# Kernel optimization log

Hardware: AMD Instinct MI355X
Metric: run time of the kernel (lower is better)

Reference implementation:

```python
import jax, jax.numpy as jnp
import numpy as np

B, D = 65536, 365

def _linp(k, fan_in, fan_out):
    # torch nn.Linear default init: U(-1/sqrt(fan_in), 1/sqrt(fan_in))
    kw, kb = jax.random.split(k)
    bound = 1.0 / np.sqrt(fan_in)
    W = jax.random.uniform(kw, (fan_in, fan_out), jnp.float32, -bound, bound)
    b = jax.random.uniform(kb, (fan_out,), jnp.float32, -bound, bound)
    return W, b

def setup_inputs() -> dict:
    key = jax.random.key(0)
    ks = jax.random.split(key, 9)
    x = jax.random.normal(ks[0], (B, D), jnp.float32)
    W1, b1 = _linp(ks[1], D, 512)
    W2, b2 = _linp(ks[2], 512, 256)
    W3, b3 = _linp(ks[3], 256, 128)
    Ws, bs = _linp(ks[4], 6, 32)
    Wc1, bc1 = _linp(ks[5], 128 + 32, 64)
    Wc2, bc2 = _linp(ks[6], 64, 32)
    Wc3, bc3 = _linp(ks[7], 32, 1)
    return dict(x=x, W1=W1, b1=b1, W2=W2, b2=b2, W3=W3, b3=b3,
                Ws=Ws, bs=bs, Wc1=Wc1, bc1=bc1, Wc2=Wc2, bc2=bc2,
                Wc3=Wc3, bc3=bc3)

def _row_stats(x):
    # fused row-wise moments: mean, std (ddof=1), min, max, skew, kurtosis
    mu = jnp.mean(x, axis=1, keepdims=True)          # [B,1]
    c = x - mu                                        # [B,D]
    var1 = jnp.sum(c * c, axis=1) / (x.shape[1] - 1)  # unbiased, matches torch.std()
    sigma = jnp.sqrt(var1)
    m3 = jnp.mean(c ** 3, axis=1)
    m4 = jnp.mean(c ** 4, axis=1)
    skew = m3 / (sigma ** 3 + 1e-8)
    kurt = m4 / (sigma ** 4 + 1e-8)
    return jnp.stack([mu[:, 0], sigma, jnp.min(x, axis=1), jnp.max(x, axis=1), skew, kurt], axis=1)

def reference(x, W1, b1, W2, b2, W3, b3, Ws, bs, Wc1, bc1, Wc2, bc2, Wc3, bc3):
    h = jax.nn.relu(x @ W1 + b1)
    h = jax.nn.relu(h @ W2 + b2)
    seq = jax.nn.relu(h @ W3 + b3)            # [B,128]
    stat = _row_stats(x) @ Ws + bs            # [B,32]
    comb = jnp.concatenate([seq, stat], axis=1)
    c = jax.nn.relu(comb @ Wc1 + bc1)
    c = jax.nn.relu(c @ Wc2 + bc2)
    out = jax.nn.sigmoid(c @ Wc3 + bc3)       # [B,1]
    return out[:, 0]
```

## Files before the change

### kernel.cpp

```cpp
#include <hip/hip_runtime.h>
#include <math.h>

typedef __attribute__((ext_vector_type(8)))  short short8;
typedef __attribute__((ext_vector_type(16))) float float16;

#define DEVI __device__ __forceinline__

DEVI short f2bf(float f) {
    unsigned u = __float_as_uint(f);
    u = (u + 0x7fffu + ((u >> 16) & 1u)) >> 16;
    return (short)u;
}
DEVI unsigned pk2(float a, float b) {
    return (unsigned)(unsigned short)f2bf(a) | ((unsigned)(unsigned short)f2bf(b) << 16);
}
DEVI float16 mfma16(short8 a, short8 b, float16 c) {
    return __builtin_amdgcn_mfma_f32_32x32x16_bf16(a, b, c, 0, 0, 0);
}
DEVI int rowof(int r, int h) { return (r & 3) + 8 * (r >> 2) + 4 * h; }
DEVI short8 lds8(const short* p) { return *(const short8*)p; }
DEVI short8 gld8(const short* p) { return *(const short8*)p; }

#define W1T_OFF  0
#define W2T_OFF  188416
#define W3T_OFF  319488
#define WC1T_OFF 352256
#define WC2T_OFF 362496

__global__ void prep_v2(const float* __restrict__ W1, const float* __restrict__ W2,
                        const float* __restrict__ W3, const float* __restrict__ Wc1,
                        const float* __restrict__ Wc2, short* __restrict__ ws) {
    __shared__ short T[16 * 72];
    int b = blockIdx.x, t = threadIdx.x;
    const float* src; int K, N; size_t base; int kc, nb;
    if (b < 184)        {            src = W1;  K = 365; N = 512; base = W1T_OFF;  kc = b >> 3;  nb = b & 7; }
    else if (b < 312)   { int l = b - 184; src = W2;  K = 512; N = 256; base = W2T_OFF;  kc = l >> 2;  nb = l & 3; }
    else if (b < 344)   { int l = b - 312; src = W3;  K = 256; N = 128; base = W3T_OFF;  kc = l >> 1;  nb = l & 1; }
    else if (b < 354)   {            src = Wc1; K = 160; N = 64;  base = WC1T_OFF; kc = b - 344; nb = 0; }
    else                {            src = Wc2; K = 64;  N = 32;  base = WC2T_OFF; kc = b - 354; nb = 0; }
    int n = nb * 64 + (t & 63);
    int kr = t >> 6;
    #pragma unroll
    for (int i = 0; i < 4; ++i) {
        int krow = kr + 4 * i;
        int k = kc * 16 + krow;
        float v = (k < K && n < N) ? src[(size_t)k * N + n] : 0.f;
        T[krow * 72 + (t & 63)] = f2bf(v);
    }
    __syncthreads();
    int n2 = t >> 2, ksq = (t & 3) * 4;
    int ng = nb * 64 + n2;
    if (ng < N) {
        unsigned lo = (unsigned)(unsigned short)T[ksq * 72 + n2]
                    | ((unsigned)(unsigned short)T[(ksq + 1) * 72 + n2] << 16);
        unsigned hi = (unsigned)(unsigned short)T[(ksq + 2) * 72 + n2]
                    | ((unsigned)(unsigned short)T[(ksq + 3) * 72 + n2] << 16);
        uint2 d; d.x = lo; d.y = hi;
        *(uint2*)(ws + base + ((size_t)kc * N + ng) * 16 + ksq) = d;
    }
}

__global__ __launch_bounds__(256, 2)
void fused_v5(const float* __restrict__ x,
              const float* __restrict__ b1f, const float* __restrict__ b2f,
              const float* __restrict__ b3f, const float* __restrict__ Wsf,
              const float* __restrict__ bsf, const float* __restrict__ bc1f,
              const float* __restrict__ bc2f, const float* __restrict__ Wc3f,
              const float* __restrict__ bc3f,
              const short* __restrict__ wsw, float* __restrict__ out)
{
    __shared__ __align__(16) char smem[53248];
    short* XT    = (short*)smem;
    short* SB0   = (short*)smem;
    short* SB1   = (short*)(smem + 17408);
    float* C2f   = (float*)(smem + 36864);
    short* FEATL = (short*)(smem + 48128);

    const short* W1t  = wsw + W1T_OFF;
    const short* W2t  = wsw + W2T_OFF;
    const short* W3t  = wsw + W3T_OFF;
    const short* Wc1t = wsw + WC1T_OFF;
    const short* Wc2t = wsw + WC2T_OFF;

    const int tid  = (int)threadIdx.x;
    const int lane = tid & 63;
    const int wv   = tid >> 6;
    const int m    = lane & 31;
    const int h    = lane >> 5;
    const int rowBase = (int)blockIdx.x * 64;

    float bb1[2][2], bb2[2];
    #pragma unroll
    for (int p = 0; p < 2; ++p)
    #pragma unroll
    for (int ct = 0; ct < 2; ++ct) bb1[p][ct] = b1f[256 * p + 64 * wv + 32 * ct + m];
    bb2[0] = b2f[64 * wv + m]; bb2[1] = b2f[64 * wv + 32 + m];
    float bb3  = b3f[32 * wv + m];
    float bbc1 = bc1f[32 * (wv & 1) + m];
    float bbc2 = bc2f[m];

    const int r0 = tid >> 2, q = tid & 2 ? (tid & 3) : (tid & 3);
    const int qq = tid & 3;
    const float* xrow = x + (size_t)(rowBase + r0) * 365;
    float s1 = 0.f, s2 = 0.f, s3 = 0.f, s4 = 0.f, mn = 1e30f, mx = -1e30f;
    #pragma unroll
    for (int i = 0; i < 12; ++i) {
        int o = qq + 4 * i;
        if (o <= 45) {
            float xf[8];
            #pragma unroll
            for (int jj = 0; jj < 8; ++jj) {
                int col = o * 8 + jj;
                xf[jj] = (col < 365) ? xrow[col] : 0.f;
            }
            #pragma unroll
            for (int jj = 0; jj < 8; ++jj) {
                int col = o * 8 + jj;
                if (col < 365) {
                    float v = xf[jj], v2 = v * v;
                    s1 += v; s2 += v2; s3 += v2 * v; s4 += v2 * v2;
                    mn = fminf(mn, v); mx = fmaxf(mx, v);
                }
            }
            int4 w4;
            w4.x = (int)pk2(xf[0], xf[1]); w4.y = (int)pk2(xf[2], xf[3]);
            w4.z = (int)pk2(xf[4], xf[5]); w4.w = (int)pk2(xf[6], xf[7]);
            *(int4*)(XT + r0 * 376 + o * 8) = w4;
        }
    }
    #pragma unroll
    for (int off = 1; off <= 2; off <<= 1) {
        s1 += __shfl_xor(s1, off); s2 += __shfl_xor(s2, off);
        s3 += __shfl_xor(s3, off); s4 += __shfl_xor(s4, off);
        mn = fminf(mn, __shfl_xor(mn, off)); mx = fmaxf(mx, __shfl_xor(mx, off));
    }
    {
        float mean  = s1 * (1.0f / 365.0f);
        float var1  = (s2 - 365.0f * mean * mean) * (1.0f / 364.0f);
        float sigma = sqrtf(var1);
        float m3 = (s3 - 3.0f * mean * s2) * (1.0f / 365.0f) + 2.0f * mean * mean * mean;
        float mm = mean * mean;
        float m4 = (s4 - 4.0f * mean * s3 + 6.0f * mm * s2) * (1.0f / 365.0f) - 3.0f * mm * mm;
        float sg2 = sigma * sigma;
        float skew = m3 / (sigma * sg2 + 1e-8f);
        float kurt = m4 / (sg2 * sg2 + 1e-8f);
        float st[6] = { mean, sigma, mn, mx, skew, kurt };
        float f[8];
        #pragma unroll
        for (int c0 = 0; c0 < 8; ++c0) {
            int c = 8 * qq + c0;
            float acc = bsf[c];
            #pragma unroll
            for (int jj = 0; jj < 6; ++jj) acc += st[jj] * Wsf[jj * 32 + c];
            f[c0] = acc;
        }
        int4 w4;
        w4.x = (int)pk2(f[0], f[1]); w4.y = (int)pk2(f[2], f[3]);
        w4.z = (int)pk2(f[4], f[5]); w4.w = (int)pk2(f[6], f[7]);
        *(int4*)(FEATL + r0 * 40 + 8 * qq) = w4;
    }
    __syncthreads();

    const short* Ap0 = XT + m * 376 + h * 8;
    const short* Ap1 = Ap0 + 32 * 376;
    unsigned park[2][2][2][8];
    #pragma unroll
    for (int p = 0; p < 2; ++p) {
        float16 c00, c01, c10, c11;
        #pragma unroll
        for (int i = 0; i < 16; ++i) { c00[i] = 0.f; c01[i] = 0.f; c10[i] = 0.f; c11[i] = 0.f; }
        const short* B1 = W1t + (256 * p + 64 * wv + m) * 16 + h * 8;
        #pragma unroll
        for (int kc = 0; kc < 23; ++kc) {
            short8 b0 = gld8(B1 + kc * 8192);
            short8 b1 = gld8(B1 + 512 + kc * 8192);
            short8 a0 = lds8(Ap0 + kc * 16);
            short8 a1 = lds8(Ap1 + kc * 16);
            c00 = mfma16(a0, b0, c00);
            c01 = mfma16(a1, b0, c01);
            c10 = mfma16(a0, b1, c10);
            c11 = mfma16(a1, b1, c11);
        }
        #pragma unroll
        for (int rr = 0; rr < 8; ++rr) {
            park[p][0][0][rr] = pk2(fmaxf(c00[2*rr] + bb1[p][0], 0.f), fmaxf(c00[2*rr+1] + bb1[p][0], 0.f));
            park[p][0][1][rr] = pk2(fmaxf(c01[2*rr] + bb1[p][0], 0.f), fmaxf(c01[2*rr+1] + bb1[p][0], 0.f));
            park[p][1][0][rr] = pk2(fmaxf(c10[2*rr] + bb1[p][1], 0.f), fmaxf(c10[2*rr+1] + bb1[p][1], 0.f));
            park[p][1][1][rr] = pk2(fmaxf(c11[2*rr] + bb1[p][1], 0.f), fmaxf(c11[2*rr+1] + bb1[p][1], 0.f));
        }
    }
    __syncthreads();

    float16 H00, H01, H10, H11;
    #pragma unroll
    for (int i = 0; i < 16; ++i) { H00[i] = 0.f; H01[i] = 0.f; H10[i] = 0.f; H11[i] = 0.f; }
    const short* A2r0 = SB0 + m * 136 + h * 8;
    #pragma unroll
    for (int s = 0; s < 4; ++s) {
        short* SBs = (s & 1) ? SB1 : SB0;
        if ((wv >> 1) == (s & 1)) {
            int p = s >> 1;
            int cb = 64 * (wv & 1) + m;
            #pragma unroll
            for (int ct = 0; ct < 2; ++ct)
            #pragma unroll
            for (int rt = 0; rt < 2; ++rt)
            #pragma unroll
            for (int rr = 0; rr < 8; ++rr) {
                unsigned pv = park[p][ct][rt][rr];
                int row = rt * 32 + rowof(2 * rr, h);
                SBs[row * 136 + cb + 32 * ct]       = (short)(pv & 0xffffu);
                SBs[(row + 1) * 136 + cb + 32 * ct] = (short)(pv >> 16);
            }
        }
        __syncthreads();
        const short* A0p = SBs + m * 136 + h * 8;
        const short* A1p = A0p + 32 * 136;
        const short* B2 = W2t + (64 * wv + m) * 16 + h * 8 + s * 32768;
        #pragma unroll
        for (int i = 0; i < 8; ++i) {
            short8 b0 = gld8(B2 + i * 4096);
            short8 b1 = gld8(B2 + 512 + i * 4096);
            short8 a0 = lds8(A0p + i * 16);
            short8 a1 = lds8(A1p + i * 16);
            H00 = mfma16(a0, b0, H00);
            H01 = mfma16(a1, b0, H01);
            H10 = mfma16(a0, b1, H10);
            H11 = mfma16(a1, b1, H11);
        }
    }
    (void)A2r0;

    float16 S0, S1;
    #pragma unroll
    for (int i = 0; i < 16; ++i) { S0[i] = 0.f; S1[i] = 0.f; }
    #pragma unroll
    for (int t = 0; t < 2; ++t) {
        short* SBs = t ? SB1 : SB0;
        if ((wv >> 1) == t) {
            int cb = 64 * (wv & 1) + m;
            #pragma unroll
            for (int rr = 0; rr < 8; ++rr) {
                int rw0 = rowof(2 * rr, h);
                SBs[rw0 * 136 + cb]              = f2bf(fmaxf(H00[2*rr]   + bb2[0], 0.f));
                SBs[(rw0 + 1) * 136 + cb]        = f2bf(fmaxf(H00[2*rr+1] + bb2[0], 0.f));
                SBs[(32 + rw0) * 136 + cb]       = f2bf(fmaxf(H01[2*rr]   + bb2[0], 0.f));
                SBs[(33 + rw0) * 136 + cb]       = f2bf(fmaxf(H01[2*rr+1] + bb2[0], 0.f));
                SBs[rw0 * 136 + cb + 32]         = f2bf(fmaxf(H10[2*rr]   + bb2[1], 0.f));
                SBs[(rw0 + 1) * 136 + cb + 32]   = f2bf(fmaxf(H10[2*rr+1] + bb2[1], 0.f));
                SBs[(32 + rw0) * 136 + cb + 32]  = f2bf(fmaxf(H11[2*rr]   + bb2[1], 0.f));
                SBs[(33 + rw0) * 136 + cb + 32]  = f2bf(fmaxf(H11[2*rr+1] + bb2[1], 0.f));
            }
        }
        __syncthreads();
        const short* A0p = SBs + m * 136 + h * 8;
        const short* A1p = A0p + 32 * 136;
        const short* B3 = W3t + (32 * wv + m) * 16 + h * 8 + t * 16384;
        #pragma unroll
        for (int i = 0; i < 8; ++i) {
            short8 b  = gld8(B3 + i * 2048);
            short8 a0 = lds8(A0p + i * 16);
            short8 a1 = lds8(A1p + i * 16);
            S0 = mfma16(a0, b, S0);
            S1 = mfma16(a1, b, S1);
        }
    }

    {
        int cb = 32 * wv + m;
        #pragma unroll
        for (int rr = 0; rr < 8; ++rr) {
            int rw0 = rowof(2 * rr, h);
            SB0[rw0 * 136 + cb]        = f2bf(fmaxf(S0[2*rr]   + bb3, 0.f));
            SB0[(rw0 + 1) * 136 + cb]  = f2bf(fmaxf(S0[2*rr+1] + bb3, 0.f));
            SB0[(32 + rw0) * 136 + cb] = f2bf(fmaxf(S1[2*rr]   + bb3, 0.f));
            SB0[(33 + rw0) * 136 + cb] = f2bf(fmaxf(S1[2*rr+1] + bb3, 0.f));
        }
    }
    __syncthreads();

    {
        int rt4 = wv >> 1, c4 = wv & 1;
        float16 g4;
        #pragma unroll
        for (int i = 0; i < 16; ++i) g4[i] = 0.f;
        const short* A4 = SB0 + (rt4 * 32 + m) * 136 + h * 8;
        const short* B4 = Wc1t + (32 * c4 + m) * 16 + h * 8;
        #pragma unroll
        for (int i = 0; i < 8; ++i)
            g4 = mfma16(lds8(A4 + i * 16), gld8(B4 + i * 1024), g4);
        const short* AF = FEATL + (rt4 * 32 + m) * 40 + h * 8;
        #pragma unroll
        for (int i = 0; i < 2; ++i)
            g4 = mfma16(lds8(AF + i * 16), gld8(B4 + (8 + i) * 1024), g4);
        short* C1 = SB1;
        #pragma unroll
        for (int r = 0; r < 16; ++r)
            C1[(rt4 * 32 + rowof(r, h)) * 72 + 32 * c4 + m] = f2bf(fmaxf(g4[r] + bbc1, 0.f));
    }
    __syncthreads();

    if (wv < 2) {
        const short* A5 = SB1 + (32 * wv + m) * 72 + h * 8;
        const short* B5 = Wc2t + m * 16 + h * 8;
        float16 g5;
        #pragma unroll
        for (int i = 0; i < 16; ++i) g5[i] = 0.f;
        #pragma unroll
        for (int i = 0; i < 4; ++i)
            g5 = mfma16(lds8(A5 + i * 16), gld8(B5 + i * 512), g5);
        #pragma unroll
        for (int r = 0; r < 16; ++r)
            C2f[(32 * wv + rowof(r, h)) * 33 + m] = fmaxf(g5[r] + bbc2, 0.f);
    }
    __syncthreads();

    if (tid < 64) {
        float z = bc3f[0];
        #pragma unroll
        for (int i = 0; i < 32; ++i) z += C2f[tid * 33 + i] * Wc3f[i];
        out[rowBase + tid] = 1.0f / (1.0f + expf(-z));
    }
}

extern "C" void kernel_launch(void* const* d_in, const int* in_sizes, int n_in,
                              void* d_out, int out_size, void* d_ws, size_t ws_size,
                              hipStream_t stream)
{
    (void)in_sizes; (void)n_in; (void)out_size; (void)ws_size;
    const float* x   = (const float*)d_in[0];
    const float* W1  = (const float*)d_in[1];
    const float* b1  = (const float*)d_in[2];
    const float* W2  = (const float*)d_in[3];
    const float* b2  = (const float*)d_in[4];
    const float* W3  = (const float*)d_in[5];
    const float* b3  = (const float*)d_in[6];
    const float* Ws  = (const float*)d_in[7];
    const float* bs  = (const float*)d_in[8];
    const float* Wc1 = (const float*)d_in[9];
    const float* bc1 = (const float*)d_in[10];
    const float* Wc2 = (const float*)d_in[11];
    const float* bc2 = (const float*)d_in[12];
    const float* Wc3 = (const float*)d_in[13];
    const float* bc3 = (const float*)d_in[14];
    short* ws = (short*)d_ws;

    prep_v2<<<358, 256, 0, stream>>>(W1, W2, W3, Wc1, Wc2, ws);
    fused_v5<<<1024, 256, 0, stream>>>(x, b1, b2, b3, Ws, bs, bc1, bc2, Wc3, bc3,
                                       ws, (float*)d_out);
}
```

Baseline: 245.5 us.

## Coalesce x row loads per wave and raise occupancy bound to three blocks

Replaces the per-thread strided load of x (four threads per row, each reading eight scalar columns) with a per-wave scheme in which each wave handles 16 rows and lanes read consecutive columns. Loads are therefore coalesced, and row moments are reduced with a full 64-lane shuffle tree. The bf16 packing now uses a neighbour shuffle, and the stat projection computes one output column per lane. The launch bound also rises from 2 to 3 blocks per SM, which gives more latency hiding but may force register spills given the large park/accumulator arrays.

```diff
diff --git a/kernel.cpp b/kernel.cpp
--- a/kernel.cpp
+++ b/kernel.cpp
@@ -60,8 +60,8 @@
     }
 }
 
-__global__ __launch_bounds__(256, 2)
-void fused_v5(const float* __restrict__ x,
+__global__ __launch_bounds__(256, 3)
+void fused_v6(const float* __restrict__ x,
               const float* __restrict__ b1f, const float* __restrict__ b2f,
               const float* __restrict__ b3f, const float* __restrict__ Wsf,
               const float* __restrict__ bsf, const float* __restrict__ bc1f,
@@ -98,43 +98,50 @@
     float bb3  = b3f[32 * wv + m];
     float bbc1 = bc1f[32 * (wv & 1) + m];
     float bbc2 = bc2f[m];
-
-    const int r0 = tid >> 2, q = tid & 2 ? (tid & 3) : (tid & 3);
-    const int qq = tid & 3;
-    const float* xrow = x + (size_t)(rowBase + r0) * 365;
-    float s1 = 0.f, s2 = 0.f, s3 = 0.f, s4 = 0.f, mn = 1e30f, mx = -1e30f;
-    #pragma unroll
-    for (int i = 0; i < 12; ++i) {
-        int o = qq + 4 * i;
-        if (o <= 45) {
-            float xf[8];
-            #pragma unroll
-            for (int jj = 0; jj < 8; ++jj) {
-                int col = o * 8 + jj;
-                xf[jj] = (col < 365) ? xrow[col] : 0.f;
-            }
-            #pragma unroll
-            for (int jj = 0; jj < 8; ++jj) {
-                int col = o * 8 + jj;
-                if (col < 365) {
-                    float v = xf[jj], v2 = v * v;
-                    s1 += v; s2 += v2; s3 += v2 * v; s4 += v2 * v2;
-                    mn = fminf(mn, v); mx = fmaxf(mx, v);
-                }
-            }
-            int4 w4;
-            w4.x = (int)pk2(xf[0], xf[1]); w4.y = (int)pk2(xf[2], xf[3]);
-            w4.z = (int)pk2(xf[4], xf[5]); w4.w = (int)pk2(xf[6], xf[7]);
-            *(int4*)(XT + r0 * 376 + o * 8) = w4;
-        }
-    }
-    #pragma unroll
-    for (int off = 1; off <= 2; off <<= 1) {
-        s1 += __shfl_xor(s1, off); s2 += __shfl_xor(s2, off);
-        s3 += __shfl_xor(s3, off); s4 += __shfl_xor(s4, off);
-        mn = fminf(mn, __shfl_xor(mn, off)); mx = fmaxf(mx, __shfl_xor(mx, off));
-    }
-    {
+    float wsf[6], bsl = bsf[m];
+    #pragma unroll
+    for (int j = 0; j < 6; ++j) wsf[j] = Wsf[j * 32 + m];
+
+    #pragma unroll
+    for (int i = 0; i < 16; ++i) {
+        int r = wv * 16 + i;
+        const float* xr = x + (size_t)(rowBase + r) * 365;
+        float v[6];
+        #pragma unroll
+        for (int t = 0; t < 5; ++t) v[t] = xr[64 * t + lane];
+        v[5] = (lane < 45) ? xr[320 + lane] : 0.f;
+
+        float s1 = 0.f, s2 = 0.f, s3 = 0.f, s4 = 0.f, mnr = 1e30f, mxr = -1e30f;
+        #pragma unroll
+        for (int t = 0; t < 5; ++t) {
+            float vv = v[t], v2 = vv * vv;
+            s1 += vv; s2 += v2; s3 += v2 * vv; s4 += v2 * v2;
+            mnr = fminf(mnr, vv); mxr = fmaxf(mxr, vv);
+        }
+        {
+            float vv = v[5], v2 = vv * vv;
+            s1 += vv; s2 += v2; s3 += v2 * vv; s4 += v2 * v2;
+            if (lane < 45) { mnr = fminf(mnr, vv); mxr = fmaxf(mxr, vv); }
+        }
+        unsigned pv[6];
+        #pragma unroll
+        for (int t = 0; t < 6; ++t) {
+            float vh = __shfl_xor(v[t], 1);
+            pv[t] = pk2(v[t], vh);
+        }
+        if (!(lane & 1)) {
+            #pragma unroll
+            for (int t = 0; t < 5; ++t)
+                *(unsigned*)(XT + r * 376 + t * 64 + lane) = pv[t];
+            if (lane <= 46)
+                *(unsigned*)(XT + r * 376 + 320 + lane) = pv[5];
+        }
+        #pragma unroll
+        for (int off = 1; off <= 32; off <<= 1) {
+            s1 += __shfl_xor(s1, off); s2 += __shfl_xor(s2, off);
+            s3 += __shfl_xor(s3, off); s4 += __shfl_xor(s4, off);
+            mnr = fminf(mnr, __shfl_xor(mnr, off)); mxr = fmaxf(mxr, __shfl_xor(mxr, off));
+        }
         float mean  = s1 * (1.0f / 365.0f);
         float var1  = (s2 - 365.0f * mean * mean) * (1.0f / 364.0f);
         float sigma = sqrtf(var1);
@@ -144,20 +151,11 @@
         float sg2 = sigma * sigma;
         float skew = m3 / (sigma * sg2 + 1e-8f);
         float kurt = m4 / (sg2 * sg2 + 1e-8f);
-        float st[6] = { mean, sigma, mn, mx, skew, kurt };
-        float f[8];
-        #pragma unroll
-        for (int c0 = 0; c0 < 8; ++c0) {
-            int c = 8 * qq + c0;
-            float acc = bsf[c];
-            #pragma unroll
-            for (int jj = 0; jj < 6; ++jj) acc += st[jj] * Wsf[jj * 32 + c];
-            f[c0] = acc;
-        }
-        int4 w4;
-        w4.x = (int)pk2(f[0], f[1]); w4.y = (int)pk2(f[2], f[3]);
-        w4.z = (int)pk2(f[4], f[5]); w4.w = (int)pk2(f[6], f[7]);
-        *(int4*)(FEATL + r0 * 40 + 8 * qq) = w4;
+        if (h == 0) {
+            float f = bsl + mean * wsf[0] + sigma * wsf[1] + mnr * wsf[2]
+                          + mxr * wsf[3] + skew * wsf[4] + kurt * wsf[5];
+            FEATL[r * 40 + m] = f2bf(f);
+        }
     }
     __syncthreads();
 
@@ -194,7 +192,6 @@
     float16 H00, H01, H10, H11;
     #pragma unroll
     for (int i = 0; i < 16; ++i) { H00[i] = 0.f; H01[i] = 0.f; H10[i] = 0.f; H11[i] = 0.f; }
-    const short* A2r0 = SB0 + m * 136 + h * 8;
     #pragma unroll
     for (int s = 0; s < 4; ++s) {
         short* SBs = (s & 1) ? SB1 : SB0;
@@ -207,10 +204,10 @@
             for (int rt = 0; rt < 2; ++rt)
             #pragma unroll
             for (int rr = 0; rr < 8; ++rr) {
-                unsigned pv = park[p][ct][rt][rr];
+                unsigned pvv = park[p][ct][rt][rr];
                 int row = rt * 32 + rowof(2 * rr, h);
-                SBs[row * 136 + cb + 32 * ct]       = (short)(pv & 0xffffu);
-                SBs[(row + 1) * 136 + cb + 32 * ct] = (short)(pv >> 16);
+                SBs[row * 136 + cb + 32 * ct]       = (short)(pvv & 0xffffu);
+                SBs[(row + 1) * 136 + cb + 32 * ct] = (short)(pvv >> 16);
             }
         }
         __syncthreads();
@@ -229,7 +226,6 @@
             H11 = mfma16(a1, b1, H11);
         }
     }
-    (void)A2r0;
 
     float16 S0, S1;
     #pragma unroll
@@ -346,6 +342,6 @@
     short* ws = (short*)d_ws;
 
     prep_v2<<<358, 256, 0, stream>>>(W1, W2, W3, Wc1, Wc2, ws);
-    fused_v5<<<1024, 256, 0, stream>>>(x, b1, b2, b3, Ws, bs, bc1, bc2, Wc3, bc3,
+    fused_v6<<<1024, 256, 0, stream>>>(x, b1, b2, b3, Ws, bs, bc1, bc2, Wc3, bc3,
                                        ws, (float*)d_out);
 }
```

After: 337.0 us. 1.37x slower.
